# Kernel optimization log

Measured on AMD Instinct MI355X. Metric: run time of the kernel, lower is better.

## Reference

```python
import jax, jax.numpy as jnp
import numpy as np
import math

B, T = 8, 16
CODE_NUM = 1024
CODE_SIZE = 48
GRAPH_SIZE = 32
HIDDEN = 150      # hidden_size == t_output_size
T_ATTN = 32       # t_attention_size
DP_ATTN = 32      # DotProductAttention size
OUT = 1024


def _lin(k, fan_in, fan_out):
    s = 1.0 / math.sqrt(fan_in)
    kw, kb = jax.random.split(k)
    W = jax.random.uniform(kw, (fan_in, fan_out), minval=-s, maxval=s, dtype=jnp.float32)
    b = jax.random.uniform(kb, (fan_out,), minval=-s, maxval=s, dtype=jnp.float32)
    return W, b


def setup_inputs():
    key = jax.random.key(0)
    ks = jax.random.split(key, 16)
    u = jax.random.uniform(ks[0], (B, T, CODE_NUM))
    m1 = (u < 0.03).astype(jnp.float32)                   # persistent codes
    m2 = ((u >= 0.03) & (u < 0.05)).astype(jnp.float32)   # emerging neighbor codes
    m3 = ((u >= 0.05) & (u < 0.06)).astype(jnp.float32)   # emerging unrelated codes
    divided = jnp.stack([m1, m2, m3], axis=-1)            # [B,T,N,3], disjoint
    code_x = jnp.clip(m1 + m2 + m3, 0.0, 1.0)             # current-visit codes
    neighbors = ((u >= 0.06) & (u < 0.12)).astype(jnp.float32)
    lens = jax.random.randint(ks[1], (B,), T // 2, T + 1)
    a = (jax.random.uniform(ks[2], (CODE_NUM, CODE_NUM)) < 0.01).astype(jnp.float32)
    adj = a / (a.sum(axis=1, keepdims=True) + 1e-6)
    c_emb = jax.random.normal(ks[3], (CODE_NUM, CODE_SIZE)) * 0.05
    n_emb = jax.random.normal(ks[4], (CODE_NUM, CODE_SIZE)) * 0.05
    u_emb = jax.random.normal(ks[5], (CODE_NUM, GRAPH_SIZE)) * 0.05
    Wg, bg = _lin(ks[6], CODE_SIZE, GRAPH_SIZE)           # GraphLayer dense
    Wi, bi = _lin(ks[7], GRAPH_SIZE, 3 * HIDDEN)          # GRUCell input (r|z|n)
    Wh, bh = _lin(ks[8], HIDDEN, 3 * HIDDEN)              # GRUCell hidden (r|z|n)
    Wq, bq = _lin(ks[9], GRAPH_SIZE, T_ATTN)
    Wk, bk = _lin(ks[10], GRAPH_SIZE, T_ATTN)
    Wv, bv = _lin(ks[11], GRAPH_SIZE, HIDDEN)
    Wd, bd = _lin(ks[12], HIDDEN, DP_ATTN)                # DotProductAttention dense
    context = jax.random.normal(ks[13], (DP_ATTN,)) * 0.1
    Wc, bc = _lin(ks[14], HIDDEN, OUT)                    # Classifier
    return dict(code_x=code_x, divided=divided, neighbors=neighbors, lens=lens,
                adj=adj, c_emb=c_emb, n_emb=n_emb, u_emb=u_emb, Wg=Wg, bg=bg,
                Wi=Wi, bi=bi, Wh=Wh, bh=bh, Wq=Wq, bq=bq, Wk=Wk, bk=bk,
                Wv=Wv, bv=bv, Wd=Wd, bd=bd, context=context, Wc=Wc, bc=bc)


def _forward(code_x, divided, neighbors, lens, adj, c_emb, n_emb, u_emb,
             Wg, bg, Wi, bi, Wh, bh, Wq, bq, Wk, bk, Wv, bv, Wd, bd, context, Wc, bc):
    Bb, Tt, N = code_x.shape
    H = Wh.shape[0]
    NEG = -1e30
    scale = 1.0 / math.sqrt(Wq.shape[1])

    def step(carry, xs):
        h_prev, no_prev = carry                 # [B,N,H], [B,N,G]
        c_t, d_t, n_t, t_idx = xs               # [B,N], [B,N,3], [B,N], scalar
        c = c_t[..., None]
        nb = n_t[..., None]
        # GraphLayer: masked embeddings + one-hop adjacency aggregation
        ce = c * c_emb                           # [B,N,C]
        ne = nb * n_emb
        adj_ce = jnp.einsum('mn,bnc->bmc', adj, ce)
        adj_ne = jnp.einsum('mn,bnc->bmc', adj, ne)
        co = jax.nn.leaky_relu((ce + c * adj_ce + c * adj_ne) @ Wg + bg)      # [B,N,G]
        no = jax.nn.leaky_relu((ne + nb * adj_ne + nb * adj_ce) @ Wg + bg)

        m1 = d_t[..., 0]; m2 = d_t[..., 1]; m3 = d_t[..., 2]
        # TransitionLayer part 1: GRUCell on persistent (m1) codes; h_new starts at 0
        gi = co @ Wi + bi
        gh = h_prev @ Wh + bh
        i_r, i_z, i_n = jnp.split(gi, 3, axis=-1)
        h_r, h_z, h_n = jnp.split(gh, 3, axis=-1)
        r = jax.nn.sigmoid(i_r + h_r)
        z = jax.nn.sigmoid(i_z + h_z)
        n_g = jnp.tanh(i_n + r * h_n)
        h_m1 = (1.0 - z) * n_g + z * h_prev
        h_new = jnp.where(m1[..., None] > 0, h_m1, 0.0)

        # TransitionLayer part 2: single-head attention over emerging (m2|m3) codes, t>0
        m23 = (m2 + m3) > 0
        qrows = jnp.where(m2[..., None] > 0, no_prev,
                          jnp.where(m3[..., None] > 0, u_emb, 0.0))           # [B,N,G]
        q = qrows @ Wq + bq
        k = co @ Wk + bk
        v = qrows @ Wv + bv
        s = jnp.einsum('bia,bja->bij', q, k) * scale
        s = jnp.where(m23[:, None, :], s, NEG)   # keys restricted to m2|m3 set
        h_m23 = jnp.tanh(jnp.einsum('bij,bjh->bih', jax.nn.softmax(s, axis=-1), v))
        use23 = t_idx > 0
        h_new = jnp.where(jnp.logical_and(use23, m23)[..., None], h_m23, h_new)

        # per-step output: max-pool over each active subset (0 if subset empty)
        om1 = jnp.max(jnp.where(m1[..., None] > 0, h_m1, NEG), axis=1)
        om1 = jnp.where(jnp.any(m1 > 0, axis=1)[:, None], om1, 0.0)
        om23 = jnp.max(jnp.where(m23[..., None], h_m23, NEG), axis=1)
        om23 = jnp.where(jnp.logical_and(use23, jnp.any(m23, axis=1))[:, None], om23, 0.0)
        return (h_new, no), om1 + om23

    h0 = jnp.zeros((Bb, N, H), code_x.dtype)
    no0 = jnp.zeros((Bb, N, Wg.shape[1]), code_x.dtype)
    xs = (jnp.moveaxis(code_x, 1, 0), jnp.moveaxis(divided, 1, 0),
          jnp.moveaxis(neighbors, 1, 0), jnp.arange(Tt))
    _, outs = jax.lax.scan(step, (h0, no0), xs)
    outs = jnp.moveaxis(outs, 0, 1)              # [B,T,H]

    # DotProductAttention over (ragged) visit axis
    vu = (outs @ Wd + bd) @ context              # [B,T]
    tmask = jnp.arange(Tt)[None, :] < lens[:, None]
    score = jax.nn.softmax(jnp.where(tmask, vu, NEG), axis=-1)
    pooled = jnp.einsum('bth,bt->bh', outs, score)
    # Classifier (dropout_rate=0 -> identity) with sigmoid activation
    return jax.nn.sigmoid(pooled @ Wc + bc)


def reference(code_x, divided, neighbors, lens, adj, c_emb, n_emb, u_emb,
              Wg, bg, Wi, bi, Wh, bh, Wq, bq, Wk, bk, Wv, bv, Wd, bd, context, Wc, bc):
    return _forward(code_x, divided, neighbors, lens, adj, c_emb, n_emb, u_emb,
                    Wg, bg, Wi, bi, Wh, bh, Wq, bq, Wk, bk, Wv, bv, Wd, bd,
                    context, Wc, bc)
```

## Files before the change

### kernel.cpp

```cpp
#include <hip/hip_runtime.h>
#include <hip/hip_bf16.h>

#define Bq   8
#define Tq   16
#define Nq   1024
#define Cq   48
#define Gq   32
#define Hq   150
#define H3q  450
#define TAq  32
#define OUTq 1024
#define BTq  128

#define NC_CAP 128
#define NM_CAP 64
#define NACT   (2 * NC_CAP)
#define MTILE  16
#define NMH    (NM_CAP / 2)

__device__ __forceinline__ float lrelu(float x){ return x > 0.f ? x : 0.01f * x; }
__device__ __forceinline__ float sigm(float x){ return 1.f / (1.f + expf(-x)); }

__device__ int   g_n1[BTq], g_n23[BTq], g_nchain[BTq], g_nchain2[BTq];
__device__ short g_list1[BTq][NM_CAP];
__device__ short g_list23[BTq][NM_CAP];
__device__ short g_mapc[BTq][Nq];
__device__ short g_mapn[BTq][Nq];
__device__ int   g_chain[BTq][NM_CAP];
__device__ int   g_chain2[BTq][NM_CAP];
__device__ unsigned char g_cls[BTq][NM_CAP];
__device__ float g_Pc[Nq][Gq];
__device__ float g_Pn[Nq][Gq];
__device__ float g_co[BTq][NC_CAP][Gq];
__device__ float g_no[BTq][NC_CAP][Gq];
__device__ float g_hm23[BTq][NM_CAP][Hq];
__device__ float g_om23p2[2][BTq][Hq];
__device__ float g_hm1[BTq][NM_CAP][Hq];
__device__ float g_om1p2[2][BTq][Hq];
__device__ float g_om1c[BTq][Hq];

__device__ __forceinline__ void gi3(const float* co_row, const float* Wi, const float* bi, int h,
                                    float& gr, float& gz, float& gn){
    gr = bi[h]; gz = bi[Hq + h]; gn = bi[2 * Hq + h];
    #pragma unroll
    for (int g = 0; g < Gq; ++g){
        float c = co_row[g];
        const float* w = Wi + g * H3q + h;
        gr += c * w[0];
        gz += c * w[Hq];
        gn += c * w[2 * Hq];
    }
}

__global__ __launch_bounds__(256) void k_pre(const float* c_emb, const float* n_emb, const float* Wg){
    int idx   = blockIdx.x * 256 + threadIdx.x;
    int which = idx >> 15;
    int r     = (idx >> 5) & 1023;
    int g     = idx & 31;
    const float* emb = which ? n_emb : c_emb;
    float acc = 0.f;
    for (int c = 0; c < Cq; ++c)
        acc += emb[r * Cq + c] * Wg[c * Gq + g];
    if (which) g_Pn[r][g] = acc; else g_Pc[r][g] = acc;
}

__global__ __launch_bounds__(512) void k_co(const float* code_x, const float* neighbors,
                                            const float* adj, const float* bg){
    int bt = blockIdx.x >> 1, half = blockIdx.x & 1, tid = threadIdx.x;
    __shared__ short lc_s[NC_CAP], ln_s[NC_CAP];
    __shared__ short act_s[NACT];
    __shared__ int nc_s, nn_s;
    __shared__ float Pact_s[NACT][Gq];
    __shared__ float A_s[MTILE][NACT];
    __shared__ short mrow_s[MTILE];
    int wave = tid >> 6, lane = tid & 63;

    if (wave == 0){
        int base = 0;
        for (int start = 0; start < Nq; start += 64){
            int n = start + lane;
            int pred = code_x[bt * Nq + n] > 0.f;
            unsigned long long mm = __ballot(pred);
            int pos = base + (int)__popcll(mm & ((1ull << lane) - 1ull));
            if (pred && pos < NC_CAP) lc_s[pos] = (short)n;
            base += (int)__popcll(mm);
        }
        if (lane == 0) nc_s = min(base, NC_CAP);
    } else if (wave == 1){
        int base = 0;
        for (int start = 0; start < Nq; start += 64){
            int n = start + lane;
            int pred = neighbors[bt * Nq + n] > 0.f;
            unsigned long long mm = __ballot(pred);
            int pos = base + (int)__popcll(mm & ((1ull << lane) - 1ull));
            if (pred && pos < NC_CAP) ln_s[pos] = (short)n;
            base += (int)__popcll(mm);
        }
        if (lane == 0) nn_s = min(base, NC_CAP);
    } else {
        if (half == 0) for (int n = tid - 128; n < Nq; n += 384) g_mapc[bt][n] = -1;
        else           for (int n = tid - 128; n < Nq; n += 384) g_mapn[bt][n] = -1;
    }
    __syncthreads();
    int nc = nc_s, nn = nn_s, total = nc + nn;

    for (int i = tid; i < total; i += 512) act_s[i] = (i < nc) ? lc_s[i] : ln_s[i - nc];
    if (half == 0) for (int i = tid; i < nc; i += 512) g_mapc[bt][lc_s[i]] = (short)i;
    else           for (int i = tid; i < nn; i += 512) g_mapn[bt][ln_s[i]] = (short)i;
    __syncthreads();

    for (int idx = tid; idx < total * Gq; idx += 512){
        int i = idx >> 5, g = idx & 31;
        Pact_s[i][g] = (i < nc) ? g_Pc[act_s[i]][g] : g_Pn[act_s[i]][g];
    }
    __syncthreads();

    int g = tid & 31, grp = tid >> 5;
    float bgv = bg[g];
    for (int rbase = half; rbase < total; rbase += 2 * MTILE){
        if (tid < MTILE){
            int r = rbase + 2 * tid;
            mrow_s[tid] = (r < total) ? act_s[r] : 0;
        }
        __syncthreads();
        int ntile = min(MTILE, (total - rbase + 1) / 2);
        for (int idx = tid; idx < ntile * total; idx += 512){
            int ti = idx / total, j = idx % total;
            A_s[ti][j] = adj[(size_t)mrow_s[ti] * Nq + act_s[j]];
        }
        __syncthreads();
        if (grp < ntile){
            int r = rbase + 2 * grp;
            float agg = 0.f;
            #pragma unroll 4
            for (int j = 0; j < total; ++j) agg += A_s[grp][j] * Pact_s[j][g];
            float v = lrelu(Pact_s[r][g] + agg + bgv);
            if (r < nc) g_co[bt][r][g]      = v;
            else        g_no[bt][r - nc][g] = v;
        }
        __syncthreads();
    }
}

__global__ __launch_bounds__(512) void k_mid(const float* divided, const float* u_emb,
                                             const float* Wk, const float* bk,
                                             const float* Wq_, const float* bq_,
                                             const float* Wv_, const float* bv_,
                                             const float* bg){
    int bt = blockIdx.x >> 1, half = blockIdx.x & 1, tid = threadIdx.x;
    int t = bt % Tq, btp = bt - 1;
    __shared__ unsigned char f1_s[Nq], f2_s[Nq], f3_s[Nq];
    __shared__ short l1_s[NM_CAP], l23_s[NM_CAP];
    __shared__ unsigned char wm_s[NMH];
    __shared__ int n1_s, n23_s;
    __shared__ float co23_s[NM_CAP][Gq];
    __shared__ float qr_s[NM_CAP][Gq];
    __shared__ float q_s[NMH][TAq + 1];
    __shared__ float k_s[NM_CAP][TAq + 1];
    __shared__ float s_s[NMH][NM_CAP + 1];
    __shared__ float vv_s[NM_CAP][Hq];
    __shared__ float hm_s[NMH][Hq];
    int wave = tid >> 6, lane = tid & 63;

    for (int idx = tid; idx < Nq * 3; idx += 512){
        float v = divided[(size_t)bt * Nq * 3 + idx];
        int n = idx / 3, c = idx - n * 3;
        unsigned char f = (v > 0.f) ? 1 : 0;
        if (c == 0) f1_s[n] = f;
        else if (c == 1) f2_s[n] = f;
        else f3_s[n] = f;
    }
    __syncthreads();
    if (wave == 0){
        int base = 0;
        for (int start = 0; start < Nq; start += 64){
            int n = start + lane;
            int pred = f1_s[n];
            unsigned long long mm = __ballot(pred != 0);
            int pos = base + (int)__popcll(mm & ((1ull << lane) - 1ull));
            if (pred && pos < NM_CAP) l1_s[pos] = (short)n;
            base += (int)__popcll(mm);
        }
        if (lane == 0) n1_s = min(base, NM_CAP);
    } else if (wave == 1){
        int base = 0;
        for (int start = 0; start < Nq; start += 64){
            int n = start + lane;
            int m2 = f2_s[n], m3 = f3_s[n];
            int pred = m2 | m3;
            unsigned long long mm = __ballot(pred != 0);
            int pos = base + (int)__popcll(mm & ((1ull << lane) - 1ull));
            if (pred && pos < NM_CAP) l23_s[pos] = (short)(n | (m2 ? 0x400 : 0));
            base += (int)__popcll(mm);
        }
        if (lane == 0) n23_s = min(base, NM_CAP);
    }
    __syncthreads();
    int n1 = n1_s, n23 = n23_s;
    if (half == 0){
        for (int i = tid; i < n1;  i += 512) g_list1[bt][i]  = l1_s[i];
        for (int i = tid; i < n23; i += 512) g_list23[bt][i] = l23_s[i];
        if (tid == 0){ g_n1[bt] = n1; g_n23[bt] = n23; }
    }
    if (t == 0 || n23 == 0) return;
    int nMy = (n23 > half) ? ((n23 - half + 1) >> 1) : 0;

    for (int il = tid; il < nMy; il += 512){
        int row = l23_s[2 * il + half] & 1023;
        unsigned char wm = 0;
        if (t < Tq - 1) wm = (divided[((size_t)(bt + 1) * Nq + row) * 3] > 0.f) ? 1 : 0;
        wm_s[il] = wm;
    }
    for (int idx = tid; idx < n23 * Gq; idx += 512){
        int i = idx >> 5, g = idx & 31;
        co23_s[i][g] = g_co[bt][g_mapc[bt][l23_s[i] & 1023]][g];
    }
    for (int idx = tid; idx < n23 * Gq; idx += 512){
        int i = idx >> 5, g = idx & 31;
        int e = l23_s[i], row = e & 1023;
        float qv;
        if (e & 0x400){
            int slot = g_mapn[btp][row];
            qv = (slot >= 0) ? g_no[btp][slot][g] : lrelu(bg[g]);
        } else {
            qv = u_emb[row * Gq + g];
        }
        qr_s[i][g] = qv;
    }
    __syncthreads();
    for (int idx = tid; idx < n23 * TAq; idx += 512){
        int i = idx >> 5, a = idx & 31;
        float acck = bk[a];
        #pragma unroll
        for (int g = 0; g < Gq; ++g) acck += co23_s[i][g] * Wk[g * TAq + a];
        k_s[i][a] = acck;
    }
    for (int idx = tid; idx < nMy * TAq; idx += 512){
        int il = idx >> 5, a = idx & 31;
        int i = 2 * il + half;
        float accq = bq_[a];
        #pragma unroll
        for (int g = 0; g < Gq; ++g) accq += qr_s[i][g] * Wq_[g * TAq + a];
        q_s[il][a] = accq;
    }
    for (int idx = tid; idx < n23 * Hq; idx += 512){
        int i = idx / Hq, h = idx % Hq;
        float acc = bv_[h];
        #pragma unroll
        for (int g = 0; g < Gq; ++g) acc += qr_s[i][g] * Wv_[g * Hq + h];
        vv_s[i][h] = acc;
    }
    __syncthreads();

    const float scale = 0.17677669529663687f;
    for (int idx = tid; idx < nMy * n23; idx += 512){
        int il = idx / n23, j = idx % n23;
        float acc = 0.f;
        #pragma unroll
        for (int a = 0; a < TAq; ++a) acc += q_s[il][a] * k_s[j][a];
        s_s[il][j] = acc * scale;
    }
    __syncthreads();
    for (int il = tid; il < nMy; il += 512){
        float mx = -1e30f;
        for (int j = 0; j < n23; ++j) mx = fmaxf(mx, s_s[il][j]);
        float sum = 0.f;
        for (int j = 0; j < n23; ++j){ float e = expf(s_s[il][j] - mx); s_s[il][j] = e; sum += e; }
        float inv = 1.f / sum;
        for (int j = 0; j < n23; ++j) s_s[il][j] *= inv;
    }
    __syncthreads();
    for (int idx = tid; idx < nMy * Hq; idx += 512){
        int il = idx / Hq, h = idx % Hq;
        float acc = 0.f;
        for (int j = 0; j < n23; ++j) acc += s_s[il][j] * vv_s[j][h];
        hm_s[il][h] = tanhf(acc);
    }
    __syncthreads();
    for (int idx = tid; idx < nMy * Hq; idx += 512){
        int il = idx / Hq, h = idx % Hq;
        if (wm_s[il]) g_hm23[bt][2 * il + half][h] = hm_s[il][h];
    }
    for (int h = tid; h < Hq; h += 512){
        float mx = -1e30f;
        for (int il = 0; il < nMy; ++il) mx = fmaxf(mx, hm_s[il][h]);
        g_om23p2[half][bt][h] = mx;
    }
}

__global__ __launch_bounds__(512) void k_gru1(const float* Wi, const float* bi,
                                              const float* Wh, const float* bh){
    int bt = blockIdx.x >> 1, half = blockIdx.x & 1, tid = threadIdx.x;
    int t = bt % Tq, btp = bt - 1;
    __shared__ short map1p[Nq], map23p[Nq];
    __shared__ short l1_s[NM_CAP];
    __shared__ unsigned char cls_s[NM_CAP];
    __shared__ int m23l_s[NM_CAP];
    __shared__ int nf23_s;
    __shared__ float co1_s[NMH][Gq];
    __shared__ float hb_s[Hq];
    __shared__ float ghf_s[H3q];
    __shared__ float gi_s[NMH][H3q];
    int n1 = g_n1[bt];
    int nMy = (n1 > half) ? ((n1 - half + 1) >> 1) : 0;
    for (int n = tid; n < Nq; n += 512){ map1p[n] = -1; map23p[n] = -1; }
    for (int i = tid; i < n1; i += 512) l1_s[i] = g_list1[bt][i];
    __syncthreads();
    if (t >= 1){
        int n1p = g_n1[btp];
        for (int i = tid; i < n1p; i += 512) map1p[g_list1[btp][i]] = (short)i;
        if (t >= 2){
            int n23p = g_n23[btp];
            for (int i = tid; i < n23p; i += 512) map23p[g_list23[btp][i] & 1023] = (short)i;
        }
    }
    __syncthreads();
    if (tid < 64){
        int i = tid;
        int cls = 0, sp = -1;
        if (i < n1 && t >= 1){
            int row = l1_s[i];
            if (map1p[row] >= 0){ cls = 1; sp = map1p[row]; }
            else if (t >= 2 && map23p[row] >= 0){ cls = 2; sp = map23p[row]; }
        }
        if (i < n1) cls_s[i] = (unsigned char)cls;
        if (half == 0 && i < n1) g_cls[bt][i] = (unsigned char)cls;
        unsigned long long mch = __ballot(cls == 1);
        unsigned long long m23 = __ballot(cls == 2 && (i & 1) == half);
        int pch = (int)__popcll(mch & ((1ull << i) - 1ull));
        int p23 = (int)__popcll(m23 & ((1ull << i) - 1ull));
        if (half == 0 && cls == 1) g_chain[bt][pch] = (i << 16) | sp;
        if (cls == 2 && (i & 1) == half) m23l_s[p23] = (i << 16) | sp;
        if (i == 0){
            nf23_s = (int)__popcll(m23);
            if (half == 0) g_nchain[bt] = (int)__popcll(mch);
        }
    }
    for (int idx = tid; idx < nMy * Gq; idx += 512){
        int il = idx >> 5, g = idx & 31;
        co1_s[il][g] = g_co[bt][g_mapc[bt][l1_s[2 * il + half]]][g];
    }
    __syncthreads();

    if (tid < H3q){
        float wcol[Gq];
        #pragma unroll
        for (int g = 0; g < Gq; ++g) wcol[g] = Wi[g * H3q + tid];
        float bij = bi[tid];
        for (int il = 0; il < nMy; ++il){
            float acc = bij;
            #pragma unroll
            for (int g = 0; g < Gq; ++g) acc += co1_s[il][g] * wcol[g];
            gi_s[il][tid] = acc;
        }
    }
    __syncthreads();

    for (int idx = tid; idx < nMy * Hq; idx += 512){
        int il = idx / Hq, h = idx % Hq;
        int i = 2 * il + half;
        if (cls_s[i] != 0) continue;
        float gr = gi_s[il][h], gz = gi_s[il][Hq + h], gn = gi_s[il][2 * Hq + h];
        float r  = sigm(gr + bh[h]);
        float z  = sigm(gz + bh[Hq + h]);
        float ng = tanhf(gn + r * bh[2 * Hq + h]);
        gi_s[il][h] = (1.f - z) * ng;
    }
    __syncthreads();

    int nf23 = nf23_s;
    for (int f = 0; f < nf23; ++f){
        int pk = m23l_s[f]; int i = pk >> 16, sp = pk & 0xffff;
        int il = i >> 1;
        for (int h = tid; h < Hq; h += 512) hb_s[h] = g_hm23[btp][sp][h];
        __syncthreads();
        for (int j = tid; j < H3q; j += 512){
            float acc = bh[j];
            for (int k2 = 0; k2 < Hq; ++k2) acc += hb_s[k2] * Wh[k2 * H3q + j];
            ghf_s[j] = acc;
        }
        __syncthreads();
        for (int h = tid; h < Hq; h += 512){
            float gr = gi_s[il][h], gz = gi_s[il][Hq + h], gn = gi_s[il][2 * Hq + h];
            float r  = sigm(gr + ghf_s[h]);
            float z  = sigm(gz + ghf_s[Hq + h]);
            float ng = tanhf(gn + r * ghf_s[2 * Hq + h]);
            gi_s[il][h] = (1.f - z) * ng + z * hb_s[h];
        }
        __syncthreads();
    }

    for (int idx = tid; idx < nMy * Hq; idx += 512){
        int il = idx / Hq, h = idx % Hq;
        int i = 2 * il + half;
        if (cls_s[i] != 1) g_hm1[bt][i][h] = gi_s[il][h];
    }
    for (int h = tid; h < Hq; h += 512){
        float mx = -1e30f;
        for (int il = 0; il < nMy; ++il)
            if (cls_s[2 * il + half] != 1) mx = fmaxf(mx, gi_s[il][h]);
        g_om1p2[half][bt][h] = mx;
    }
}

__global__ __launch_bounds__(512) void k_gru1b(const float* Wi, const float* bi,
                                               const float* Wh, const float* bh){
    int bt = blockIdx.x, tid = threadIdx.x;
    int t = bt % Tq, btp = bt - 1;
    __shared__ unsigned char defer_s[NM_CAP];
    __shared__ float co_s[Gq];
    __shared__ float hb_s[Hq];
    __shared__ float ghf_s[H3q];
    __shared__ float cmax_s[Hq];
    int nch = (t > 0) ? g_nchain[bt] : 0;
    for (int h = tid; h < Hq; h += 512) cmax_s[h] = -1e30f;
    if (tid < 64){
        int c = tid;
        int defer = 0;
        if (c < nch){
            int sp = g_chain[bt][c] & 0xffff;
            defer = (g_cls[btp][sp] == 1) ? 1 : 0;
            defer_s[c] = (unsigned char)defer;
        }
        unsigned long long md = __ballot((c < nch) && defer);
        int pos = (int)__popcll(md & ((1ull << c) - 1ull));
        if ((c < nch) && defer) g_chain2[bt][pos] = g_chain[bt][c];
        if (c == 0) g_nchain2[bt] = (int)__popcll(md);
    }
    __syncthreads();
    for (int c = 0; c < nch; ++c){
        if (defer_s[c]) continue;
        int pk = g_chain[bt][c]; int i = pk >> 16, sp = pk & 0xffff;
        if (tid < Gq) co_s[tid] = g_co[bt][g_mapc[bt][g_list1[bt][i]]][tid];
        for (int h = tid; h < Hq; h += 512) hb_s[h] = g_hm1[btp][sp][h];
        __syncthreads();
        for (int j = tid; j < H3q; j += 512){
            float acc = bh[j];
            for (int k2 = 0; k2 < Hq; ++k2) acc += hb_s[k2] * Wh[k2 * H3q + j];
            ghf_s[j] = acc;
        }
        __syncthreads();
        for (int h = tid; h < Hq; h += 512){
            float gr, gz, gn;
            gi3(co_s, Wi, bi, h, gr, gz, gn);
            float r  = sigm(gr + ghf_s[h]);
            float z  = sigm(gz + ghf_s[Hq + h]);
            float ng = tanhf(gn + r * ghf_s[2 * Hq + h]);
            float v  = (1.f - z) * ng + z * hb_s[h];
            g_hm1[bt][i][h] = v;
            cmax_s[h] = fmaxf(cmax_s[h], v);
        }
        __syncthreads();
    }
    for (int h = tid; h < Hq; h += 512) g_om1c[bt][h] = cmax_s[h];
}

__global__ __launch_bounds__(512) void k_gru2f(const float* Wi, const float* bi,
                                               const float* Wh, const float* bh,
                                               const int* lens, const float* Wd, const float* bd,
                                               const float* ctx, const float* Wc, const float* bc,
                                               float* out){
    int b = blockIdx.x, tid = threadIdx.x;
    __shared__ float co_s[Gq];
    __shared__ float hb_s[Hq];
    __shared__ float ghf_s[H3q];
    __shared__ float outs_s[Tq][Hq];
    __shared__ float wdc_s[Hq];
    __shared__ float score_s[Tq];
    __shared__ float pooled_s[Hq];
    for (int t = 1; t < Tq; ++t){
        int bt = b * Tq + t, btp = bt - 1;
        int nch2 = g_nchain2[bt];
        for (int c = 0; c < nch2; ++c){
            int pk = g_chain2[bt][c]; int i = pk >> 16, sp = pk & 0xffff;
            if (tid < Gq) co_s[tid] = g_co[bt][g_mapc[bt][g_list1[bt][i]]][tid];
            for (int h = tid; h < Hq; h += 512) hb_s[h] = g_hm1[btp][sp][h];
            __syncthreads();
            for (int j = tid; j < H3q; j += 512){
                float acc = bh[j];
                for (int k2 = 0; k2 < Hq; ++k2) acc += hb_s[k2] * Wh[k2 * H3q + j];
                ghf_s[j] = acc;
            }
            __syncthreads();
            for (int h = tid; h < Hq; h += 512){
                float gr, gz, gn;
                gi3(co_s, Wi, bi, h, gr, gz, gn);
                float r  = sigm(gr + ghf_s[h]);
                float z  = sigm(gz + ghf_s[Hq + h]);
                float ng = tanhf(gn + r * ghf_s[2 * Hq + h]);
                g_hm1[bt][i][h] = (1.f - z) * ng + z * hb_s[h];
            }
            __syncthreads();
        }
    }
    for (int idx = tid; idx < Tq * Hq; idx += 512){
        int t = idx / Hq, h = idx % Hq;
        int bt = b * Tq + t;
        int n1 = g_n1[bt], n23 = (t > 0) ? g_n23[bt] : 0;
        float o = 0.f;
        if (n1 > 0){
            float mx = fmaxf(fmaxf(g_om1p2[0][bt][h], g_om1p2[1][bt][h]), g_om1c[bt][h]);
            int nd = (t > 0) ? g_nchain2[bt] : 0;
            for (int c = 0; c < nd; ++c){
                int i = g_chain2[bt][c] >> 16;
                mx = fmaxf(mx, g_hm1[bt][i][h]);
            }
            o = mx;
        }
        if (n23 > 0) o += fmaxf(g_om23p2[0][bt][h], g_om23p2[1][bt][h]);
        outs_s[t][h] = o;
    }
    for (int h = tid; h < Hq; h += 512){
        float acc = 0.f;
        for (int d = 0; d < 32; ++d) acc += Wd[h * 32 + d] * ctx[d];
        wdc_s[h] = acc;
    }
    __syncthreads();
    int len = lens[b];
    if (tid < Tq){
        int t = tid;
        float acc = 0.f;
        for (int d = 0; d < 32; ++d) acc += bd[d] * ctx[d];
        for (int h = 0; h < Hq; ++h) acc += outs_s[t][h] * wdc_s[h];
        score_s[t] = (t < len) ? acc : -1e30f;
    }
    __syncthreads();
    if (tid == 0){
        float mx = -1e30f;
        for (int t = 0; t < Tq; ++t) mx = fmaxf(mx, score_s[t]);
        float sum = 0.f;
        for (int t = 0; t < Tq; ++t){ float e = expf(score_s[t] - mx); score_s[t] = e; sum += e; }
        float inv = 1.f / sum;
        for (int t = 0; t < Tq; ++t) score_s[t] *= inv;
    }
    __syncthreads();
    for (int h = tid; h < Hq; h += 512){
        float acc = 0.f;
        for (int t = 0; t < Tq; ++t) acc += score_s[t] * outs_s[t][h];
        pooled_s[h] = acc;
    }
    __syncthreads();
    for (int o = tid; o < OUTq; o += 512){
        float acc = bc[o];
        for (int h = 0; h < Hq; ++h) acc += pooled_s[h] * Wc[h * OUTq + o];
        out[b * OUTq + o] = sigm(acc);
    }
}

extern "C" void kernel_launch(void* const* d_in, const int* in_sizes, int n_in,
                              void* d_out, int out_size, void* d_ws, size_t ws_size,
                              hipStream_t stream){
    const float* code_x    = (const float*)d_in[0];
    const float* divided   = (const float*)d_in[1];
    const float* neighbors = (const float*)d_in[2];
    const int*   lens      = (const int*)  d_in[3];
    const float* adj       = (const float*)d_in[4];
    const float* c_emb     = (const float*)d_in[5];
    const float* n_emb     = (const float*)d_in[6];
    const float* u_emb     = (const float*)d_in[7];
    const float* Wg        = (const float*)d_in[8];
    const float* bg        = (const float*)d_in[9];
    const float* Wi        = (const float*)d_in[10];
    const float* bi        = (const float*)d_in[11];
    const float* Wh        = (const float*)d_in[12];
    const float* bh        = (const float*)d_in[13];
    const float* Wq_       = (const float*)d_in[14];
    const float* bq_       = (const float*)d_in[15];
    const float* Wk_       = (const float*)d_in[16];
    const float* bk_       = (const float*)d_in[17];
    const float* Wv_       = (const float*)d_in[18];
    const float* bv_       = (const float*)d_in[19];
    const float* Wd_       = (const float*)d_in[20];
    const float* bd_       = (const float*)d_in[21];
    const float* ctx       = (const float*)d_in[22];
    const float* Wc_       = (const float*)d_in[23];
    const float* bc_       = (const float*)d_in[24];
    float* out = (float*)d_out;

    hipLaunchKernelGGL(k_pre,   dim3(256),     dim3(256), 0, stream, c_emb, n_emb, Wg);
    hipLaunchKernelGGL(k_co,    dim3(2 * BTq), dim3(512), 0, stream, code_x, neighbors, adj, bg);
    hipLaunchKernelGGL(k_mid,   dim3(2 * BTq), dim3(512), 0, stream, divided, u_emb,
                       Wk_, bk_, Wq_, bq_, Wv_, bv_, bg);
    hipLaunchKernelGGL(k_gru1,  dim3(2 * BTq), dim3(512), 0, stream, Wi, bi, Wh, bh);
    hipLaunchKernelGGL(k_gru1b, dim3(BTq),     dim3(512), 0, stream, Wi, bi, Wh, bh);
    hipLaunchKernelGGL(k_gru2f, dim3(Bq),      dim3(512), 0, stream, Wi, bi, Wh, bh,
                       lens, Wd_, bd_, ctx, Wc_, bc_, out);
}
```

Measured before the change: 264.7 us.

## Fuse embedding projection into k_co and split per-visit work across four blocks

Removes the k_pre launch by computing the embedding-times-Wg projection only for active codes inside k_co, with Wg staged in shared memory. Splits k_co, k_mid and k_gru1 across four blocks per visit instead of two, so the partial max reductions become four-way. It also caches the code flags in shared memory and drops the co23 staging buffer in favour of direct global reads. This trades one fewer launch and more parallelism for redundant list-building and projection work in each block.

```diff
diff --git a/kernel.cpp b/kernel.cpp
--- a/kernel.cpp
+++ b/kernel.cpp
@@ -16,7 +16,7 @@
 #define NM_CAP 64
 #define NACT   (2 * NC_CAP)
 #define MTILE  16
-#define NMH    (NM_CAP / 2)
+#define NMQ    (NM_CAP / 4)
 
 __device__ __forceinline__ float lrelu(float x){ return x > 0.f ? x : 0.01f * x; }
 __device__ __forceinline__ float sigm(float x){ return 1.f / (1.f + expf(-x)); }
@@ -29,14 +29,12 @@
 __device__ int   g_chain[BTq][NM_CAP];
 __device__ int   g_chain2[BTq][NM_CAP];
 __device__ unsigned char g_cls[BTq][NM_CAP];
-__device__ float g_Pc[Nq][Gq];
-__device__ float g_Pn[Nq][Gq];
 __device__ float g_co[BTq][NC_CAP][Gq];
 __device__ float g_no[BTq][NC_CAP][Gq];
 __device__ float g_hm23[BTq][NM_CAP][Hq];
-__device__ float g_om23p2[2][BTq][Hq];
+__device__ float g_om23p4[4][BTq][Hq];
 __device__ float g_hm1[BTq][NM_CAP][Hq];
-__device__ float g_om1p2[2][BTq][Hq];
+__device__ float g_om1p4[4][BTq][Hq];
 __device__ float g_om1c[BTq][Hq];
 
 __device__ __forceinline__ void gi3(const float* co_row, const float* Wi, const float* bi, int h,
@@ -52,21 +50,12 @@
     }
 }
 
-__global__ __launch_bounds__(256) void k_pre(const float* c_emb, const float* n_emb, const float* Wg){
-    int idx   = blockIdx.x * 256 + threadIdx.x;
-    int which = idx >> 15;
-    int r     = (idx >> 5) & 1023;
-    int g     = idx & 31;
-    const float* emb = which ? n_emb : c_emb;
-    float acc = 0.f;
-    for (int c = 0; c < Cq; ++c)
-        acc += emb[r * Cq + c] * Wg[c * Gq + g];
-    if (which) g_Pn[r][g] = acc; else g_Pc[r][g] = acc;
-}
-
 __global__ __launch_bounds__(512) void k_co(const float* code_x, const float* neighbors,
-                                            const float* adj, const float* bg){
-    int bt = blockIdx.x >> 1, half = blockIdx.x & 1, tid = threadIdx.x;
+                                            const float* adj, const float* Wg, const float* bg,
+                                            const float* c_emb, const float* n_emb){
+    int bt = blockIdx.x >> 2, quarter = blockIdx.x & 3, tid = threadIdx.x;
+    __shared__ unsigned char cf_s[Nq], nf_s[Nq];
+    __shared__ float Wg_s[Cq][Gq];
     __shared__ short lc_s[NC_CAP], ln_s[NC_CAP];
     __shared__ short act_s[NACT];
     __shared__ int nc_s, nn_s;
@@ -75,12 +64,20 @@
     __shared__ short mrow_s[MTILE];
     int wave = tid >> 6, lane = tid & 63;
 
+    for (int n = tid; n < Nq; n += 512){
+        cf_s[n] = (code_x[bt * Nq + n]    > 0.f) ? 1 : 0;
+        nf_s[n] = (neighbors[bt * Nq + n] > 0.f) ? 1 : 0;
+    }
+    for (int idx = tid; idx < Cq * Gq; idx += 512) (&Wg_s[0][0])[idx] = Wg[idx];
+    if (quarter == 0) for (int n = tid; n < Nq; n += 512) g_mapc[bt][n] = -1;
+    if (quarter == 1) for (int n = tid; n < Nq; n += 512) g_mapn[bt][n] = -1;
+    __syncthreads();
     if (wave == 0){
         int base = 0;
         for (int start = 0; start < Nq; start += 64){
             int n = start + lane;
-            int pred = code_x[bt * Nq + n] > 0.f;
-            unsigned long long mm = __ballot(pred);
+            int pred = cf_s[n];
+            unsigned long long mm = __ballot(pred != 0);
             int pos = base + (int)__popcll(mm & ((1ull << lane) - 1ull));
             if (pred && pos < NC_CAP) lc_s[pos] = (short)n;
             base += (int)__popcll(mm);
@@ -90,47 +87,47 @@
         int base = 0;
         for (int start = 0; start < Nq; start += 64){
             int n = start + lane;
-            int pred = neighbors[bt * Nq + n] > 0.f;
-            unsigned long long mm = __ballot(pred);
+            int pred = nf_s[n];
+            unsigned long long mm = __ballot(pred != 0);
             int pos = base + (int)__popcll(mm & ((1ull << lane) - 1ull));
             if (pred && pos < NC_CAP) ln_s[pos] = (short)n;
             base += (int)__popcll(mm);
         }
         if (lane == 0) nn_s = min(base, NC_CAP);
-    } else {
-        if (half == 0) for (int n = tid - 128; n < Nq; n += 384) g_mapc[bt][n] = -1;
-        else           for (int n = tid - 128; n < Nq; n += 384) g_mapn[bt][n] = -1;
     }
     __syncthreads();
     int nc = nc_s, nn = nn_s, total = nc + nn;
-
     for (int i = tid; i < total; i += 512) act_s[i] = (i < nc) ? lc_s[i] : ln_s[i - nc];
-    if (half == 0) for (int i = tid; i < nc; i += 512) g_mapc[bt][lc_s[i]] = (short)i;
-    else           for (int i = tid; i < nn; i += 512) g_mapn[bt][ln_s[i]] = (short)i;
-    __syncthreads();
-
+    __syncthreads();
+    if (quarter == 0) for (int i = tid; i < nc; i += 512) g_mapc[bt][lc_s[i]] = (short)i;
+    if (quarter == 1) for (int i = tid; i < nn; i += 512) g_mapn[bt][ln_s[i]] = (short)i;
     for (int idx = tid; idx < total * Gq; idx += 512){
         int i = idx >> 5, g = idx & 31;
-        Pact_s[i][g] = (i < nc) ? g_Pc[act_s[i]][g] : g_Pn[act_s[i]][g];
+        int row = act_s[i];
+        const float* emb = (i < nc) ? (c_emb + (size_t)row * Cq) : (n_emb + (size_t)row * Cq);
+        float acc = 0.f;
+        #pragma unroll
+        for (int c = 0; c < Cq; ++c) acc += emb[c] * Wg_s[c][g];
+        Pact_s[i][g] = acc;
     }
     __syncthreads();
 
     int g = tid & 31, grp = tid >> 5;
     float bgv = bg[g];
-    for (int rbase = half; rbase < total; rbase += 2 * MTILE){
+    for (int rbase = quarter; rbase < total; rbase += 4 * MTILE){
         if (tid < MTILE){
-            int r = rbase + 2 * tid;
+            int r = rbase + 4 * tid;
             mrow_s[tid] = (r < total) ? act_s[r] : 0;
         }
         __syncthreads();
-        int ntile = min(MTILE, (total - rbase + 1) / 2);
+        int ntile = min(MTILE, (total - rbase + 3) >> 2);
         for (int idx = tid; idx < ntile * total; idx += 512){
             int ti = idx / total, j = idx % total;
             A_s[ti][j] = adj[(size_t)mrow_s[ti] * Nq + act_s[j]];
         }
         __syncthreads();
         if (grp < ntile){
-            int r = rbase + 2 * grp;
+            int r = rbase + 4 * grp;
             float agg = 0.f;
             #pragma unroll 4
             for (int j = 0; j < total; ++j) agg += A_s[grp][j] * Pact_s[j][g];
@@ -147,19 +144,18 @@
                                              const float* Wq_, const float* bq_,
                                              const float* Wv_, const float* bv_,
                                              const float* bg){
-    int bt = blockIdx.x >> 1, half = blockIdx.x & 1, tid = threadIdx.x;
+    int bt = blockIdx.x >> 2, quarter = blockIdx.x & 3, tid = threadIdx.x;
     int t = bt % Tq, btp = bt - 1;
     __shared__ unsigned char f1_s[Nq], f2_s[Nq], f3_s[Nq];
     __shared__ short l1_s[NM_CAP], l23_s[NM_CAP];
-    __shared__ unsigned char wm_s[NMH];
+    __shared__ unsigned char wm_s[NMQ];
     __shared__ int n1_s, n23_s;
-    __shared__ float co23_s[NM_CAP][Gq];
     __shared__ float qr_s[NM_CAP][Gq];
-    __shared__ float q_s[NMH][TAq + 1];
+    __shared__ float q_s[NMQ][TAq + 1];
     __shared__ float k_s[NM_CAP][TAq + 1];
-    __shared__ float s_s[NMH][NM_CAP + 1];
+    __shared__ float s_s[NMQ][NM_CAP + 1];
     __shared__ float vv_s[NM_CAP][Hq];
-    __shared__ float hm_s[NMH][Hq];
+    __shared__ float hm_s[NMQ][Hq];
     int wave = tid >> 6, lane = tid & 63;
 
     for (int idx = tid; idx < Nq * 3; idx += 512){
@@ -197,23 +193,19 @@
     }
     __syncthreads();
     int n1 = n1_s, n23 = n23_s;
-    if (half == 0){
+    if (quarter == 0){
         for (int i = tid; i < n1;  i += 512) g_list1[bt][i]  = l1_s[i];
         for (int i = tid; i < n23; i += 512) g_list23[bt][i] = l23_s[i];
         if (tid == 0){ g_n1[bt] = n1; g_n23[bt] = n23; }
     }
     if (t == 0 || n23 == 0) return;
-    int nMy = (n23 > half) ? ((n23 - half + 1) >> 1) : 0;
+    int nMy = (n23 > quarter) ? ((n23 - quarter + 3) >> 2) : 0;
 
     for (int il = tid; il < nMy; il += 512){
-        int row = l23_s[2 * il + half] & 1023;
+        int row = l23_s[4 * il + quarter] & 1023;
         unsigned char wm = 0;
         if (t < Tq - 1) wm = (divided[((size_t)(bt + 1) * Nq + row) * 3] > 0.f) ? 1 : 0;
         wm_s[il] = wm;
-    }
-    for (int idx = tid; idx < n23 * Gq; idx += 512){
-        int i = idx >> 5, g = idx & 31;
-        co23_s[i][g] = g_co[bt][g_mapc[bt][l23_s[i] & 1023]][g];
     }
     for (int idx = tid; idx < n23 * Gq; idx += 512){
         int i = idx >> 5, g = idx & 31;
@@ -230,14 +222,15 @@
     __syncthreads();
     for (int idx = tid; idx < n23 * TAq; idx += 512){
         int i = idx >> 5, a = idx & 31;
+        const float* corow = g_co[bt][g_mapc[bt][l23_s[i] & 1023]];
         float acck = bk[a];
         #pragma unroll
-        for (int g = 0; g < Gq; ++g) acck += co23_s[i][g] * Wk[g * TAq + a];
+        for (int g = 0; g < Gq; ++g) acck += corow[g] * Wk[g * TAq + a];
         k_s[i][a] = acck;
     }
     for (int idx = tid; idx < nMy * TAq; idx += 512){
         int il = idx >> 5, a = idx & 31;
-        int i = 2 * il + half;
+        int i = 4 * il + quarter;
         float accq = bq_[a];
         #pragma unroll
         for (int g = 0; g < Gq; ++g) accq += qr_s[i][g] * Wq_[g * TAq + a];
@@ -279,30 +272,30 @@
     __syncthreads();
     for (int idx = tid; idx < nMy * Hq; idx += 512){
         int il = idx / Hq, h = idx % Hq;
-        if (wm_s[il]) g_hm23[bt][2 * il + half][h] = hm_s[il][h];
+        if (wm_s[il]) g_hm23[bt][4 * il + quarter][h] = hm_s[il][h];
     }
     for (int h = tid; h < Hq; h += 512){
         float mx = -1e30f;
         for (int il = 0; il < nMy; ++il) mx = fmaxf(mx, hm_s[il][h]);
-        g_om23p2[half][bt][h] = mx;
+        g_om23p4[quarter][bt][h] = mx;
     }
 }
 
 __global__ __launch_bounds__(512) void k_gru1(const float* Wi, const float* bi,
                                               const float* Wh, const float* bh){
-    int bt = blockIdx.x >> 1, half = blockIdx.x & 1, tid = threadIdx.x;
+    int bt = blockIdx.x >> 2, quarter = blockIdx.x & 3, tid = threadIdx.x;
     int t = bt % Tq, btp = bt - 1;
     __shared__ short map1p[Nq], map23p[Nq];
     __shared__ short l1_s[NM_CAP];
     __shared__ unsigned char cls_s[NM_CAP];
     __shared__ int m23l_s[NM_CAP];
     __shared__ int nf23_s;
-    __shared__ float co1_s[NMH][Gq];
+    __shared__ float co1_s[NMQ][Gq];
     __shared__ float hb_s[Hq];
     __shared__ float ghf_s[H3q];
-    __shared__ float gi_s[NMH][H3q];
+    __shared__ float gi_s[NMQ][H3q];
     int n1 = g_n1[bt];
-    int nMy = (n1 > half) ? ((n1 - half + 1) >> 1) : 0;
+    int nMy = (n1 > quarter) ? ((n1 - quarter + 3) >> 2) : 0;
     for (int n = tid; n < Nq; n += 512){ map1p[n] = -1; map23p[n] = -1; }
     for (int i = tid; i < n1; i += 512) l1_s[i] = g_list1[bt][i];
     __syncthreads();
@@ -324,21 +317,21 @@
             else if (t >= 2 && map23p[row] >= 0){ cls = 2; sp = map23p[row]; }
         }
         if (i < n1) cls_s[i] = (unsigned char)cls;
-        if (half == 0 && i < n1) g_cls[bt][i] = (unsigned char)cls;
+        if (quarter == 0 && i < n1) g_cls[bt][i] = (unsigned char)cls;
         unsigned long long mch = __ballot(cls == 1);
-        unsigned long long m23 = __ballot(cls == 2 && (i & 1) == half);
+        unsigned long long m23 = __ballot(cls == 2 && (i & 3) == quarter);
         int pch = (int)__popcll(mch & ((1ull << i) - 1ull));
         int p23 = (int)__popcll(m23 & ((1ull << i) - 1ull));
-        if (half == 0 && cls == 1) g_chain[bt][pch] = (i << 16) | sp;
-        if (cls == 2 && (i & 1) == half) m23l_s[p23] = (i << 16) | sp;
+        if (quarter == 0 && cls == 1) g_chain[bt][pch] = (i << 16) | sp;
+        if (cls == 2 && (i & 3) == quarter) m23l_s[p23] = (i << 16) | sp;
         if (i == 0){
             nf23_s = (int)__popcll(m23);
-            if (half == 0) g_nchain[bt] = (int)__popcll(mch);
+            if (quarter == 0) g_nchain[bt] = (int)__popcll(mch);
         }
     }
     for (int idx = tid; idx < nMy * Gq; idx += 512){
         int il = idx >> 5, g = idx & 31;
-        co1_s[il][g] = g_co[bt][g_mapc[bt][l1_s[2 * il + half]]][g];
+        co1_s[il][g] = g_co[bt][g_mapc[bt][l1_s[4 * il + quarter]]][g];
     }
     __syncthreads();
 
@@ -358,7 +351,7 @@
 
     for (int idx = tid; idx < nMy * Hq; idx += 512){
         int il = idx / Hq, h = idx % Hq;
-        int i = 2 * il + half;
+        int i = 4 * il + quarter;
         if (cls_s[i] != 0) continue;
         float gr = gi_s[il][h], gz = gi_s[il][Hq + h], gn = gi_s[il][2 * Hq + h];
         float r  = sigm(gr + bh[h]);
@@ -371,7 +364,7 @@
     int nf23 = nf23_s;
     for (int f = 0; f < nf23; ++f){
         int pk = m23l_s[f]; int i = pk >> 16, sp = pk & 0xffff;
-        int il = i >> 1;
+        int il = i >> 2;
         for (int h = tid; h < Hq; h += 512) hb_s[h] = g_hm23[btp][sp][h];
         __syncthreads();
         for (int j = tid; j < H3q; j += 512){
@@ -392,14 +385,14 @@
 
     for (int idx = tid; idx < nMy * Hq; idx += 512){
         int il = idx / Hq, h = idx % Hq;
-        int i = 2 * il + half;
+        int i = 4 * il + quarter;
         if (cls_s[i] != 1) g_hm1[bt][i][h] = gi_s[il][h];
     }
     for (int h = tid; h < Hq; h += 512){
         float mx = -1e30f;
         for (int il = 0; il < nMy; ++il)
-            if (cls_s[2 * il + half] != 1) mx = fmaxf(mx, gi_s[il][h]);
-        g_om1p2[half][bt][h] = mx;
+            if (cls_s[4 * il + quarter] != 1) mx = fmaxf(mx, gi_s[il][h]);
+        g_om1p4[quarter][bt][h] = mx;
     }
 }
 
@@ -499,7 +492,9 @@
         int n1 = g_n1[bt], n23 = (t > 0) ? g_n23[bt] : 0;
         float o = 0.f;
         if (n1 > 0){
-            float mx = fmaxf(fmaxf(g_om1p2[0][bt][h], g_om1p2[1][bt][h]), g_om1c[bt][h]);
+            float mx = fmaxf(fmaxf(g_om1p4[0][bt][h], g_om1p4[1][bt][h]),
+                             fmaxf(g_om1p4[2][bt][h], g_om1p4[3][bt][h]));
+            mx = fmaxf(mx, g_om1c[bt][h]);
             int nd = (t > 0) ? g_nchain2[bt] : 0;
             for (int c = 0; c < nd; ++c){
                 int i = g_chain2[bt][c] >> 16;
@@ -507,7 +502,11 @@
             }
             o = mx;
         }
-        if (n23 > 0) o += fmaxf(g_om23p2[0][bt][h], g_om23p2[1][bt][h]);
+        if (n23 > 0){
+            float m23x = fmaxf(fmaxf(g_om23p4[0][bt][h], g_om23p4[1][bt][h]),
+                               fmaxf(g_om23p4[2][bt][h], g_om23p4[3][bt][h]));
+            o += m23x;
+        }
         outs_s[t][h] = o;
     }
     for (int h = tid; h < Hq; h += 512){
@@ -577,11 +576,11 @@
     const float* bc_       = (const float*)d_in[24];
     float* out = (float*)d_out;
 
-    hipLaunchKernelGGL(k_pre,   dim3(256),     dim3(256), 0, stream, c_emb, n_emb, Wg);
-    hipLaunchKernelGGL(k_co,    dim3(2 * BTq), dim3(512), 0, stream, code_x, neighbors, adj, bg);
-    hipLaunchKernelGGL(k_mid,   dim3(2 * BTq), dim3(512), 0, stream, divided, u_emb,
+    hipLaunchKernelGGL(k_co,    dim3(4 * BTq), dim3(512), 0, stream, code_x, neighbors, adj,
+                       Wg, bg, c_emb, n_emb);
+    hipLaunchKernelGGL(k_mid,   dim3(4 * BTq), dim3(512), 0, stream, divided, u_emb,
                        Wk_, bk_, Wq_, bq_, Wv_, bv_, bg);
-    hipLaunchKernelGGL(k_gru1,  dim3(2 * BTq), dim3(512), 0, stream, Wi, bi, Wh, bh);
+    hipLaunchKernelGGL(k_gru1,  dim3(4 * BTq), dim3(512), 0, stream, Wi, bi, Wh, bh);
     hipLaunchKernelGGL(k_gru1b, dim3(BTq),     dim3(512), 0, stream, Wi, bi, Wh, bh);
     hipLaunchKernelGGL(k_gru2f, dim3(Bq),      dim3(512), 0, stream, Wi, bi, Wh, bh,
                        lens, Wd_, bd_, ctx, Wc_, bc_, out);
```

Result: slower. 276.6 us (+4.5%).
